# Kernel tuning notes

Measured on AMD Instinct MI355X. Metric: run time of the kernel, lower is better.

The kernel has to match this reference:

```python
import jax, jax.numpy as jnp
import numpy as np

BN_EPS = 1e-5
NORM_EPS = 1e-12  # torch F.normalize eps


def setup_inputs() -> dict:
    key = jax.random.key(0)
    k0, k1, k2 = jax.random.split(key, 3)
    B, C, H, W, M = 16, 256, 64, 64, 512
    query = jax.random.normal(k0, (B, C, H, W), jnp.float32)
    mem = jax.random.normal(k1, (M, C), jnp.float32)
    mem = mem / jnp.maximum(jnp.linalg.norm(mem, axis=1, keepdims=True), NORM_EPS)
    conv_w = jax.random.normal(k2, (256, 2 * C), jnp.float32) * 0.02  # 1x1 conv: [out, in]
    bn_gamma = jnp.ones((256,), jnp.float32)
    bn_beta = jnp.zeros((256,), jnp.float32)
    return {"query": query, "mem": mem, "conv_w": conv_w,
            "bn_gamma": bn_gamma, "bn_beta": bn_beta}


def reference(query, mem, conv_w, bn_gamma, bn_beta):
    B, C, H, W = query.shape
    # F.normalize over channel dim
    q = query / jnp.maximum(jnp.linalg.norm(query, axis=1, keepdims=True), NORM_EPS)
    # permute(0,2,3,1) then flatten -> [N, C], N = B*H*W
    q = q.transpose(0, 2, 3, 1).reshape(B * H * W, C)
    # query-memory similarity [N, M]
    score = q @ mem.T
    softmax_score_query = jax.nn.softmax(score, axis=0)   # softmax over all queries
    softmax_score_memory = jax.nn.softmax(score, axis=1)  # softmax over memory slots
    # weighted read from memory bank (scores detached in original)
    concat_memory = jax.lax.stop_gradient(softmax_score_memory) @ mem  # [N, C]
    updated = jnp.concatenate([q, concat_memory], axis=1)              # [N, 2C]
    updated = updated.reshape(B, H, W, 2 * C).transpose(0, 3, 1, 2)    # [B, 2C, H, W]
    # 1x1 conv (bias=False)
    y = jnp.einsum('oc,bchw->bohw', conv_w, updated)
    # BatchNorm2d (training-mode batch statistics) + ReLU
    mean = y.mean(axis=(0, 2, 3), keepdims=True)
    var = y.var(axis=(0, 2, 3), keepdims=True)
    y = (y - mean) * jax.lax.rsqrt(var + BN_EPS)
    y = y * bn_gamma[None, :, None, None] + bn_beta[None, :, None, None]
    y = jnp.maximum(y, 0.0)
    return y, softmax_score_query, softmax_score_memory
```

## Files before the change

kernel.cpp:

```cpp
#include <hip/hip_runtime.h>
#include <math.h>

#define Bq 16
#define Cc 256
#define HW 4096
#define Mm 512
#define Nn 65536
#define Oo 256
#define Kf 768

typedef short bf16x8 __attribute__((ext_vector_type(8)));
typedef float f32x4 __attribute__((ext_vector_type(4)));
typedef unsigned short ushort_t;

__device__ __forceinline__ unsigned int bf16rne(float f) {
  unsigned int u = __float_as_uint(f);
  return (u + 0x7FFFu + ((u >> 16) & 1u)) >> 16;
}
__device__ __forceinline__ float bf16f(unsigned int h) { return __uint_as_float(h << 16); }
__device__ __forceinline__ void split2(float v0, float v1,
                                       unsigned int& hi, unsigned int& lo) {
  unsigned int h0 = bf16rne(v0), h1 = bf16rne(v1);
  hi = h0 | (h1 << 16);
  unsigned int l0 = bf16rne(v0 - bf16f(h0)), l1 = bf16rne(v1 - bf16f(h1));
  lo = l0 | (l1 << 16);
}

__global__ __launch_bounds__(256) void k_qt(const float* __restrict__ query,
                                            ushort_t* __restrict__ qhiT,
                                            ushort_t* __restrict__ qloT,
                                            const float* __restrict__ mem,
                                            ushort_t* __restrict__ memT) {
  __shared__ float T[256][36];
  __shared__ float S2[8][32];
  __shared__ float invn_s[32];
  int tid = threadIdx.x, bid = blockIdx.x;
  if (bid < 2048) {
    int n0 = bid * 32;
    int b = n0 >> 12, hw0 = n0 & 4095;
    const float* qb = query + (size_t)b * Cc * HW + hw0;
#pragma unroll
    for (int p = 0; p < 8; ++p) {
      int idx = p * 256 + tid;
      int c = idx >> 3, f4 = idx & 7;
      float4 v = *(const float4*)(qb + (size_t)c * HW + f4 * 4);
      *(float4*)&T[c][f4 * 4] = v;
    }
    __syncthreads();
    {
      int n = tid & 31, cq = tid >> 5;
      float s = 0.f;
#pragma unroll
      for (int c = 0; c < 32; ++c) { float v = T[cq * 32 + c][n]; s += v * v; }
      S2[cq][n] = s;
    }
    __syncthreads();
    if (tid < 32) {
      float s = 0.f;
#pragma unroll
      for (int q = 0; q < 8; ++q) s += S2[q][tid];
      invn_s[tid] = 1.f / fmaxf(sqrtf(s), 1e-12f);
    }
    __syncthreads();
#pragma unroll
    for (int p = 0; p < 4; ++p) {
      int idx = p * 256 + tid;
      int n = idx & 31, g = idx >> 5;
      float ivn = invn_s[n];
      unsigned int hv[4], lv[4];
#pragma unroll
      for (int h = 0; h < 4; ++h) {
        int c0 = g * 8 + h * 2;
        split2(T[c0][n] * ivn, T[c0 + 1][n] * ivn, hv[h], lv[h]);
      }
      *(uint4*)(qhiT + (size_t)(n0 + n) * 256 + g * 8) = make_uint4(hv[0], hv[1], hv[2], hv[3]);
      *(uint4*)(qloT + (size_t)(n0 + n) * 256 + g * 8) = make_uint4(lv[0], lv[1], lv[2], lv[3]);
    }
  } else {
    int r0 = (bid - 2048) * 64;
#pragma unroll
    for (int p = 0; p < 8; ++p) {
      int idx = p * 256 + tid;
      int row = idx >> 5, g = idx & 31;
      const float* src = mem + (size_t)(r0 + row) * 256 + g * 8;
      float4 a = *(const float4*)(src);
      float4 c = *(const float4*)(src + 4);
      unsigned int w0 = bf16rne(a.x) | (bf16rne(a.y) << 16);
      unsigned int w1 = bf16rne(a.z) | (bf16rne(a.w) << 16);
      unsigned int w2 = bf16rne(c.x) | (bf16rne(c.y) << 16);
      unsigned int w3 = bf16rne(c.z) | (bf16rne(c.w) << 16);
      *(uint4*)(memT + (size_t)(r0 + row) * 256 + g * 8) = make_uint4(w0, w1, w2, w3);
    }
  }
}

__global__ __launch_bounds__(256) void k_wm(const float* __restrict__ conv_w,
                                            const float* __restrict__ mem,
                                            ushort_t* __restrict__ Ahi,
                                            ushort_t* __restrict__ Alo) {
  __shared__ __align__(16) float Asm[16 * 132];
  __shared__ __align__(16) float Bsm[16 * 132];
  int tid = threadIdx.x, bid = blockIdx.x;
  if (bid >= 8) {
    int b8 = bid - 8;
#pragma unroll
    for (int p = 0; p < 8; ++p) {
      int idx = b8 * 2048 + p * 256 + tid;
      int o = idx >> 6, c4 = (idx & 63) * 4;
      float4 v = *(const float4*)(conv_w + (size_t)o * 512 + c4);
      unsigned int h0, l0, h1, l1;
      split2(v.x, v.y, h0, l0);
      split2(v.z, v.w, h1, l1);
      *(uint2*)(Ahi + (size_t)o * 768 + c4) = make_uint2(h0, h1);
      *(uint2*)(Alo + (size_t)o * 768 + c4) = make_uint2(l0, l1);
    }
    return;
  }
  int tile_o = bid & 1, tile_m = bid >> 1;
  int o0 = tile_o * 128, m0 = tile_m * 128;
  int tx = tid & 15, ty = tid >> 4;
  int akk = tid & 15, ao0 = tid >> 4;
  int bk = tid & 15, bm = tid >> 4;

  float acc[2][2][4][4];
#pragma unroll
  for (int a = 0; a < 2; ++a)
#pragma unroll
    for (int c = 0; c < 2; ++c)
#pragma unroll
      for (int i = 0; i < 4; ++i)
#pragma unroll
        for (int j = 0; j < 4; ++j) acc[a][c][i][j] = 0.f;

  for (int k0 = 0; k0 < Cc; k0 += 16) {
#pragma unroll
    for (int i = 0; i < 8; ++i) {
      int o = ao0 + i * 16;
      Asm[akk * 132 + o] = conv_w[(size_t)(o0 + o) * 512 + 256 + k0 + akk];
    }
#pragma unroll
    for (int i = 0; i < 8; ++i) {
      int m = bm + i * 16;
      Bsm[bk * 132 + m] = mem[(size_t)(m0 + m) * Cc + k0 + bk];
    }
    __syncthreads();
#pragma unroll
    for (int kk = 0; kk < 16; ++kk) {
      float4 a0 = *(const float4*)&Asm[kk * 132 + ty * 4];
      float4 a1 = *(const float4*)&Asm[kk * 132 + 64 + ty * 4];
      float4 b0 = *(const float4*)&Bsm[kk * 132 + tx * 4];
      float4 b1 = *(const float4*)&Bsm[kk * 132 + 64 + tx * 4];
      float av[2][4] = {{a0.x, a0.y, a0.z, a0.w}, {a1.x, a1.y, a1.z, a1.w}};
      float bv[2][4] = {{b0.x, b0.y, b0.z, b0.w}, {b1.x, b1.y, b1.z, b1.w}};
#pragma unroll
      for (int ib = 0; ib < 2; ++ib)
#pragma unroll
        for (int i = 0; i < 4; ++i)
#pragma unroll
          for (int jb = 0; jb < 2; ++jb)
#pragma unroll
            for (int j = 0; j < 4; ++j) acc[ib][jb][i][j] += av[ib][i] * bv[jb][j];
    }
    __syncthreads();
  }
#pragma unroll
  for (int ib = 0; ib < 2; ++ib)
#pragma unroll
    for (int i = 0; i < 4; ++i) {
      int o = o0 + ib * 64 + ty * 4 + i;
#pragma unroll
      for (int jb = 0; jb < 2; ++jb) {
        int mc = m0 + jb * 64 + tx * 4;
        unsigned int h0, l0, h1, l1;
        split2(acc[ib][jb][i][0], acc[ib][jb][i][1], h0, l0);
        split2(acc[ib][jb][i][2], acc[ib][jb][i][3], h1, l1);
        *(uint2*)(Ahi + (size_t)o * 768 + 256 + mc) = make_uint2(h0, h1);
        *(uint2*)(Alo + (size_t)o * 768 + 256 + mc) = make_uint2(l0, l1);
      }
    }
}

__global__ __launch_bounds__(256) void k_score(const ushort_t* __restrict__ qhiT,
                                               const ushort_t* __restrict__ memT,
                                               float* __restrict__ exs,
                                               float* __restrict__ rowsum,
                                               float* __restrict__ colsum) {
  __shared__ ushort_t As[128 * 64];
  __shared__ ushort_t Bs[128 * 64];
  int tid = threadIdx.x, bid = blockIdx.x;
  int m0 = (bid & 3) * 128;
  int n0 = (bid >> 2) * 128;
  int lane = tid & 63;
  int w = tid >> 6, wrow = w >> 1, wcol = w & 1;

  f32x4 acc[4][4];
#pragma unroll
  for (int i = 0; i < 4; ++i)
#pragma unroll
    for (int j = 0; j < 4; ++j)
#pragma unroll
      for (int e = 0; e < 4; ++e) acc[i][j][e] = 0.f;

  uint4* As4 = (uint4*)As;
  uint4* Bs4 = (uint4*)Bs;

  for (int kt = 0; kt < 4; ++kt) {
    int k0 = kt * 64;
#pragma unroll
    for (int p = 0; p < 4; ++p) {
      int idx = p * 256 + tid;
      int row = idx >> 3, g = idx & 7;
      int G = g ^ (row & 7);
      As4[row * 8 + G] = *(const uint4*)(qhiT + (size_t)(n0 + row) * 256 + k0 + g * 8);
      Bs4[row * 8 + G] = *(const uint4*)(memT + (size_t)(m0 + row) * 256 + k0 + g * 8);
    }
    __syncthreads();
#pragma unroll
    for (int ks = 0; ks < 2; ++ks) {
      bf16x8 a[4], b[4];
#pragma unroll
      for (int i = 0; i < 4; ++i) {
        int row = wrow * 64 + i * 16 + (lane & 15);
        int G = ((lane >> 4) + ks * 4) ^ (row & 7);
        a[i] = ((const bf16x8*)As)[row * 8 + G];
      }
#pragma unroll
      for (int j = 0; j < 4; ++j) {
        int row = wcol * 64 + j * 16 + (lane & 15);
        int G = ((lane >> 4) + ks * 4) ^ (row & 7);
        b[j] = ((const bf16x8*)Bs)[row * 8 + G];
      }
#pragma unroll
      for (int i = 0; i < 4; ++i)
#pragma unroll
        for (int j = 0; j < 4; ++j)
          acc[i][j] = __builtin_amdgcn_mfma_f32_16x16x32_bf16(a[i], b[j], acc[i][j], 0, 0, 0);
    }
    __syncthreads();
  }

  float rp[4][4], cp[4];
#pragma unroll
  for (int i = 0; i < 4; ++i)
#pragma unroll
    for (int r = 0; r < 4; ++r) rp[i][r] = 0.f;
#pragma unroll
  for (int j = 0; j < 4; ++j) cp[j] = 0.f;

#pragma unroll
  for (int i = 0; i < 4; ++i) {
#pragma unroll
    for (int r = 0; r < 4; ++r) {
      int pl = wrow * 64 + i * 16 + (lane >> 4) * 4 + r;
      float* orow = exs + (size_t)(n0 + pl) * Mm + m0;
#pragma unroll
      for (int j = 0; j < 4; ++j) {
        int sl = wcol * 64 + j * 16 + (lane & 15);
        float e = __expf(acc[i][j][r]);
        orow[sl] = e;
        rp[i][r] += e;
        cp[j] += e;
      }
    }
  }

  float* red = (float*)As;
#pragma unroll
  for (int i = 0; i < 4; ++i)
#pragma unroll
    for (int r = 0; r < 4; ++r) {
      int pl = wrow * 64 + i * 16 + (lane >> 4) * 4 + r;
      red[pl * 32 + wcol * 16 + (lane & 15)] = rp[i][r];
    }
  __syncthreads();
  if (tid < 128) {
    float s = 0.f;
#pragma unroll
    for (int x = 0; x < 32; ++x) s += red[tid * 32 + x];
    atomicAdd(&rowsum[n0 + tid], s);
  }
  __syncthreads();
#pragma unroll
  for (int j = 0; j < 4; ++j) {
    int sl = wcol * 64 + j * 16 + (lane & 15);
    red[sl * 8 + wrow * 4 + (lane >> 4)] = cp[j];
  }
  __syncthreads();
  if (tid < 128) {
    float s = 0.f;
#pragma unroll
    for (int x = 0; x < 8; ++x) s += red[tid * 8 + x];
    atomicAdd(&colsum[m0 + tid], s);
  }
}

__global__ __launch_bounds__(256) void k_conv(const ushort_t* __restrict__ Ahi,
                                              const ushort_t* __restrict__ Alo,
                                              const ushort_t* __restrict__ qhiT,
                                              const ushort_t* __restrict__ qloT,
                                              const float* __restrict__ exs,
                                              const float* __restrict__ rowsum,
                                              float* __restrict__ y,
                                              float* __restrict__ bnsum,
                                              float* __restrict__ bnsumsq) {
  __shared__ ushort_t AsH[128 * 64], AsL[128 * 64];
  __shared__ ushort_t BsH[128 * 64], BsL[128 * 64];
  __shared__ float irow[128];
  int tid = threadIdx.x, bid = blockIdx.x;
  int tile_o = bid & 1, tile_n = bid >> 1;
  int o0 = tile_o * 128, n0 = tile_n * 128;
  int b = n0 >> 12, hw0 = n0 & 4095;
  if (tid < 128) irow[tid] = 1.0f / rowsum[n0 + tid];
  int lane = tid & 63;
  int w = tid >> 6, wrow = w >> 1, wcol = w & 1;

  f32x4 acc[4][4];
#pragma unroll
  for (int i = 0; i < 4; ++i)
#pragma unroll
    for (int j = 0; j < 4; ++j)
#pragma unroll
      for (int e = 0; e < 4; ++e) acc[i][j][e] = 0.f;

  uint4* AsH4 = (uint4*)AsH;
  uint4* AsL4 = (uint4*)AsL;
  uint4* BsH4 = (uint4*)BsH;
  uint4* BsL4 = (uint4*)BsL;
  uint2* BsH2 = (uint2*)BsH;
  uint2* BsL2 = (uint2*)BsL;
  __syncthreads();

  for (int kt = 0; kt < 12; ++kt) {
    int k0 = kt * 64;
#pragma unroll
    for (int p = 0; p < 4; ++p) {
      int idx = p * 256 + tid;
      int row = idx >> 3, g = idx & 7;
      int G = g ^ (row & 7);
      size_t src = (size_t)(o0 + row) * 768 + k0 + g * 8;
      AsH4[row * 8 + G] = *(const uint4*)(Ahi + src);
      AsL4[row * 8 + G] = *(const uint4*)(Alo + src);
    }
    if (k0 < 256) {
#pragma unroll
      for (int p = 0; p < 4; ++p) {
        int idx = p * 256 + tid;
        int row = idx >> 3, g = idx & 7;
        int G = g ^ (row & 7);
        size_t src = (size_t)(n0 + row) * 256 + k0 + g * 8;
        BsH4[row * 8 + G] = *(const uint4*)(qhiT + src);
        BsL4[row * 8 + G] = *(const uint4*)(qloT + src);
      }
    } else {
#pragma unroll
      for (int p = 0; p < 8; ++p) {
        int idx = p * 256 + tid;
        int row = idx >> 4, f4 = idx & 15;
        float ir = irow[row];
        float4 v = *(const float4*)(exs + (size_t)(n0 + row) * Mm + (k0 - 256) + f4 * 4);
        unsigned int h0, l0, h1, l1;
        split2(v.x * ir, v.y * ir, h0, l0);
        split2(v.z * ir, v.w * ir, h1, l1);
        int g = f4 >> 1, half = f4 & 1;
        int G = g ^ (row & 7);
        BsH2[(row * 8 + G) * 2 + half] = make_uint2(h0, h1);
        BsL2[(row * 8 + G) * 2 + half] = make_uint2(l0, l1);
      }
    }
    __syncthreads();
#pragma unroll
    for (int ks = 0; ks < 2; ++ks) {
      bf16x8 ah[4], al[4], bh[4], bl[4];
#pragma unroll
      for (int i = 0; i < 4; ++i) {
        int row = wrow * 64 + i * 16 + (lane & 15);
        int G = ((lane >> 4) + ks * 4) ^ (row & 7);
        ah[i] = ((const bf16x8*)AsH)[row * 8 + G];
        al[i] = ((const bf16x8*)AsL)[row * 8 + G];
      }
#pragma unroll
      for (int j = 0; j < 4; ++j) {
        int row = wcol * 64 + j * 16 + (lane & 15);
        int G = ((lane >> 4) + ks * 4) ^ (row & 7);
        bh[j] = ((const bf16x8*)BsH)[row * 8 + G];
        bl[j] = ((const bf16x8*)BsL)[row * 8 + G];
      }
#pragma unroll
      for (int i = 0; i < 4; ++i)
#pragma unroll
        for (int j = 0; j < 4; ++j) {
          acc[i][j] = __builtin_amdgcn_mfma_f32_16x16x32_bf16(al[i], bh[j], acc[i][j], 0, 0, 0);
          acc[i][j] = __builtin_amdgcn_mfma_f32_16x16x32_bf16(ah[i], bl[j], acc[i][j], 0, 0, 0);
          acc[i][j] = __builtin_amdgcn_mfma_f32_16x16x32_bf16(ah[i], bh[j], acc[i][j], 0, 0, 0);
        }
    }
    __syncthreads();
  }

  float rp[4][4], rq[4][4];
#pragma unroll
  for (int i = 0; i < 4; ++i)
#pragma unroll
    for (int r = 0; r < 4; ++r) { rp[i][r] = 0.f; rq[i][r] = 0.f; }

#pragma unroll
  for (int i = 0; i < 4; ++i) {
#pragma unroll
    for (int r = 0; r < 4; ++r) {
      int pl = wrow * 64 + i * 16 + (lane >> 4) * 4 + r;
      float* orow = y + (size_t)b * Oo * HW + (size_t)(o0 + pl) * HW + hw0;
#pragma unroll
      for (int j = 0; j < 4; ++j) {
        int sl = wcol * 64 + j * 16 + (lane & 15);
        float v = acc[i][j][r];
        orow[sl] = v;
        rp[i][r] += v;
        rq[i][r] += v * v;
      }
    }
  }

  float* red = (float*)AsH;
#pragma unroll
  for (int i = 0; i < 4; ++i)
#pragma unroll
    for (int r = 0; r < 4; ++r) {
      int pl = wrow * 64 + i * 16 + (lane >> 4) * 4 + r;
      red[pl * 32 + wcol * 16 + (lane & 15)] = rp[i][r];
    }
  __syncthreads();
  if (tid < 128) {
    float s = 0.f;
#pragma unroll
    for (int x = 0; x < 32; ++x) s += red[tid * 32 + x];
    atomicAdd(&bnsum[o0 + tid], s);
  }
  __syncthreads();
#pragma unroll
  for (int i = 0; i < 4; ++i)
#pragma unroll
    for (int r = 0; r < 4; ++r) {
      int pl = wrow * 64 + i * 16 + (lane >> 4) * 4 + r;
      red[pl * 32 + wcol * 16 + (lane & 15)] = rq[i][r];
    }
  __syncthreads();
  if (tid < 128) {
    float s = 0.f;
#pragma unroll
    for (int x = 0; x < 32; ++x) s += red[tid * 32 + x];
    atomicAdd(&bnsumsq[o0 + tid], s);
  }
}

__global__ __launch_bounds__(256) void k_final(float4* __restrict__ y4,
                                               const float* __restrict__ bnsum,
                                               const float* __restrict__ bnsumsq,
                                               const float* __restrict__ gamma,
                                               const float* __restrict__ beta,
                                               float4* __restrict__ smm4,
                                               const float* __restrict__ rowsum,
                                               const float4* __restrict__ colsum4,
                                               float4* __restrict__ smq4) {
  int bid = blockIdx.x;
  if (bid < 16384) {
    int g = bid * 256 + threadIdx.x;
    int o = (g >> 10) & 255;
    float mean = bnsum[o] * (1.f / Nn);
    float var = bnsumsq[o] * (1.f / Nn) - mean * mean;
    float s = gamma[o] * rsqrtf(var + 1e-5f);
    float t = beta[o] - mean * s;
    float4 v = y4[g];
    v.x = fmaxf(v.x * s + t, 0.f);
    v.y = fmaxf(v.y * s + t, 0.f);
    v.z = fmaxf(v.z * s + t, 0.f);
    v.w = fmaxf(v.w * s + t, 0.f);
    y4[g] = v;
  } else {
    int g = (bid - 16384) * 256 + threadIdx.x;
    int n = g >> 7;
    int c4 = g & 127;
    float4 e = smm4[g];
    float4 cs = colsum4[c4];
    float irn = 1.0f / rowsum[n];
    smq4[g] = make_float4(e.x / cs.x, e.y / cs.y, e.z / cs.z, e.w / cs.w);
    smm4[g] = make_float4(e.x * irn, e.y * irn, e.z * irn, e.w * irn);
  }
}

extern "C" void kernel_launch(void* const* d_in, const int* in_sizes, int n_in,
                              void* d_out, int out_size, void* d_ws, size_t ws_size,
                              hipStream_t stream) {
  (void)in_sizes; (void)n_in; (void)out_size; (void)ws_size;
  const float* query  = (const float*)d_in[0];
  const float* mem    = (const float*)d_in[1];
  const float* conv_w = (const float*)d_in[2];
  const float* gamma  = (const float*)d_in[3];
  const float* beta   = (const float*)d_in[4];
  float* out = (float*)d_out;
  float* y   = out;
  float* smq = out + 16777216;
  float* smm = smq + 33554432;
  ushort_t* qhiT = (ushort_t*)smq;
  ushort_t* qloT = (ushort_t*)(smq + 8388608);
  ushort_t* memT = (ushort_t*)(smq + 16777216);
  ushort_t* Ahi  = (ushort_t*)(smq + 16842752);
  ushort_t* Alo  = (ushort_t*)(smq + 16941056);
  float* ws = (float*)d_ws;
  float* rowsum  = ws;
  float* colsum  = ws + 65536;
  float* bnsum   = ws + 66048;
  float* bnsumsq = ws + 66304;

  hipMemsetAsync(ws, 0, 66560 * sizeof(float), stream);

  k_qt<<<2056, 256, 0, stream>>>(query, qhiT, qloT, mem, memT);
  k_wm<<<16, 256, 0, stream>>>(conv_w, mem, Ahi, Alo);
  k_score<<<2048, 256, 0, stream>>>(qhiT, memT, smm, rowsum, colsum);
  k_conv<<<1024, 256, 0, stream>>>(Ahi, Alo, qhiT, qloT, smm, rowsum,
                                   y, bnsum, bnsumsq);
  k_final<<<49152, 256, 0, stream>>>((float4*)y, bnsum, bnsumsq, gamma, beta,
                                     (float4*)smm, rowsum,
                                     (const float4*)colsum, (float4*)smq);
}
```

Baseline: 593.8 us.

## Fuse softmax normalization into conv kernel and load MFMA operands directly from global

Intermediates (exp scores, bf16 splits) move from the output buffer into workspace. Both softmax outputs are now written inside the conv kernel (only the tile_o==0 blocks) while it is already reading the exp scores. The final kernel is reduced to the BN+ReLU pass. This removes a separate full read/write pass over the two 128 MB softmax arrays. The score kernel and the q/A operand loads in the conv kernel skip LDS staging and read bf16x8 fragments straight from global memory, which drops barriers but relies on caches for operand reuse. The launcher now returns early if the workspace is too small.

Result: slower. 702.2 us (+18.3%).

```diff
diff --git a/kernel.cpp b/kernel.cpp
--- a/kernel.cpp
+++ b/kernel.cpp
@@ -7,11 +7,22 @@
 #define Mm 512
 #define Nn 65536
 #define Oo 256
-#define Kf 768
 
 typedef short bf16x8 __attribute__((ext_vector_type(8)));
 typedef float f32x4 __attribute__((ext_vector_type(4)));
 typedef unsigned short ushort_t;
+
+#define WS_ROWSUM  0
+#define WS_COLSUM  65536
+#define WS_BNSUM   66048
+#define WS_BNSUMSQ 66304
+#define WS_EXS     66560
+#define WS_QHI     33620992
+#define WS_QLO     42009600
+#define WS_MEMT    50398208
+#define WS_AHI     50463744
+#define WS_ALO     50562048
+#define WS_TOTAL   50660352
 
 __device__ __forceinline__ unsigned int bf16rne(float f) {
   unsigned int u = __float_as_uint(f);
@@ -185,13 +196,13 @@
                                                float* __restrict__ exs,
                                                float* __restrict__ rowsum,
                                                float* __restrict__ colsum) {
-  __shared__ ushort_t As[128 * 64];
-  __shared__ ushort_t Bs[128 * 64];
+  __shared__ float red[128 * 32];
   int tid = threadIdx.x, bid = blockIdx.x;
   int m0 = (bid & 3) * 128;
   int n0 = (bid >> 2) * 128;
   int lane = tid & 63;
   int w = tid >> 6, wrow = w >> 1, wcol = w & 1;
+  int rlane = lane & 15, klane = (lane >> 4) * 8;
 
   f32x4 acc[4][4];
 #pragma unroll
@@ -201,42 +212,26 @@
 #pragma unroll
       for (int e = 0; e < 4; ++e) acc[i][j][e] = 0.f;
 
-  uint4* As4 = (uint4*)As;
-  uint4* Bs4 = (uint4*)Bs;
+  const ushort_t* qbase = qhiT + (size_t)(n0 + wrow * 64 + rlane) * 256 + klane;
+  const ushort_t* mbase = memT + (size_t)(m0 + wcol * 64 + rlane) * 256 + klane;
 
   for (int kt = 0; kt < 4; ++kt) {
-    int k0 = kt * 64;
-#pragma unroll
-    for (int p = 0; p < 4; ++p) {
-      int idx = p * 256 + tid;
-      int row = idx >> 3, g = idx & 7;
-      int G = g ^ (row & 7);
-      As4[row * 8 + G] = *(const uint4*)(qhiT + (size_t)(n0 + row) * 256 + k0 + g * 8);
-      Bs4[row * 8 + G] = *(const uint4*)(memT + (size_t)(m0 + row) * 256 + k0 + g * 8);
-    }
-    __syncthreads();
 #pragma unroll
     for (int ks = 0; ks < 2; ++ks) {
+      int k0 = kt * 64 + ks * 32;
       bf16x8 a[4], b[4];
 #pragma unroll
-      for (int i = 0; i < 4; ++i) {
-        int row = wrow * 64 + i * 16 + (lane & 15);
-        int G = ((lane >> 4) + ks * 4) ^ (row & 7);
-        a[i] = ((const bf16x8*)As)[row * 8 + G];
-      }
-#pragma unroll
-      for (int j = 0; j < 4; ++j) {
-        int row = wcol * 64 + j * 16 + (lane & 15);
-        int G = ((lane >> 4) + ks * 4) ^ (row & 7);
-        b[j] = ((const bf16x8*)Bs)[row * 8 + G];
-      }
+      for (int i = 0; i < 4; ++i)
+        a[i] = *(const bf16x8*)(qbase + (size_t)(i * 16) * 256 + k0);
+#pragma unroll
+      for (int j = 0; j < 4; ++j)
+        b[j] = *(const bf16x8*)(mbase + (size_t)(j * 16) * 256 + k0);
 #pragma unroll
       for (int i = 0; i < 4; ++i)
 #pragma unroll
         for (int j = 0; j < 4; ++j)
           acc[i][j] = __builtin_amdgcn_mfma_f32_16x16x32_bf16(a[i], b[j], acc[i][j], 0, 0, 0);
     }
-    __syncthreads();
   }
 
   float rp[4][4], cp[4];
@@ -264,7 +259,6 @@
     }
   }
 
-  float* red = (float*)As;
 #pragma unroll
   for (int i = 0; i < 4; ++i)
 #pragma unroll
@@ -300,19 +294,25 @@
                                               const ushort_t* __restrict__ qloT,
                                               const float* __restrict__ exs,
                                               const float* __restrict__ rowsum,
+                                              const float* __restrict__ colsum,
                                               float* __restrict__ y,
+                                              float* __restrict__ smm,
+                                              float* __restrict__ smq,
                                               float* __restrict__ bnsum,
                                               float* __restrict__ bnsumsq) {
-  __shared__ ushort_t AsH[128 * 64], AsL[128 * 64];
   __shared__ ushort_t BsH[128 * 64], BsL[128 * 64];
   __shared__ float irow[128];
+  __shared__ float invc[512];
   int tid = threadIdx.x, bid = blockIdx.x;
   int tile_o = bid & 1, tile_n = bid >> 1;
   int o0 = tile_o * 128, n0 = tile_n * 128;
   int b = n0 >> 12, hw0 = n0 & 4095;
   if (tid < 128) irow[tid] = 1.0f / rowsum[n0 + tid];
+  invc[tid] = 1.0f / colsum[tid];
+  invc[tid + 256] = 1.0f / colsum[tid + 256];
   int lane = tid & 63;
   int w = tid >> 6, wrow = w >> 1, wcol = w & 1;
+  int rlane = lane & 15, klane = (lane >> 4) * 8;
 
   f32x4 acc[4][4];
 #pragma unroll
@@ -322,61 +322,74 @@
 #pragma unroll
       for (int e = 0; e < 4; ++e) acc[i][j][e] = 0.f;
 
-  uint4* AsH4 = (uint4*)AsH;
-  uint4* AsL4 = (uint4*)AsL;
-  uint4* BsH4 = (uint4*)BsH;
-  uint4* BsL4 = (uint4*)BsL;
+  const ushort_t* ahB = Ahi + (size_t)(o0 + wrow * 64 + rlane) * 768 + klane;
+  const ushort_t* alB = Alo + (size_t)(o0 + wrow * 64 + rlane) * 768 + klane;
+  const ushort_t* qhB = qhiT + (size_t)(n0 + wcol * 64 + rlane) * 256 + klane;
+  const ushort_t* qlB = qloT + (size_t)(n0 + wcol * 64 + rlane) * 256 + klane;
   uint2* BsH2 = (uint2*)BsH;
   uint2* BsL2 = (uint2*)BsL;
   __syncthreads();
 
-  for (int kt = 0; kt < 12; ++kt) {
-    int k0 = kt * 64;
-#pragma unroll
-    for (int p = 0; p < 4; ++p) {
+  for (int kt = 0; kt < 4; ++kt) {
+#pragma unroll
+    for (int ks = 0; ks < 2; ++ks) {
+      int k0 = kt * 64 + ks * 32;
+      bf16x8 ah[4], al[4], bh[4], bl[4];
+#pragma unroll
+      for (int i = 0; i < 4; ++i) {
+        ah[i] = *(const bf16x8*)(ahB + (size_t)(i * 16) * 768 + k0);
+        al[i] = *(const bf16x8*)(alB + (size_t)(i * 16) * 768 + k0);
+      }
+#pragma unroll
+      for (int j = 0; j < 4; ++j) {
+        bh[j] = *(const bf16x8*)(qhB + (size_t)(j * 16) * 256 + k0);
+        bl[j] = *(const bf16x8*)(qlB + (size_t)(j * 16) * 256 + k0);
+      }
+#pragma unroll
+      for (int i = 0; i < 4; ++i)
+#pragma unroll
+        for (int j = 0; j < 4; ++j) {
+          acc[i][j] = __builtin_amdgcn_mfma_f32_16x16x32_bf16(al[i], bh[j], acc[i][j], 0, 0, 0);
+          acc[i][j] = __builtin_amdgcn_mfma_f32_16x16x32_bf16(ah[i], bl[j], acc[i][j], 0, 0, 0);
+          acc[i][j] = __builtin_amdgcn_mfma_f32_16x16x32_bf16(ah[i], bh[j], acc[i][j], 0, 0, 0);
+        }
+    }
+  }
+
+  for (int kt2 = 0; kt2 < 8; ++kt2) {
+    int kg = 256 + kt2 * 64;
+    int kc = kt2 * 64;
+#pragma unroll
+    for (int p = 0; p < 8; ++p) {
       int idx = p * 256 + tid;
-      int row = idx >> 3, g = idx & 7;
+      int row = idx >> 4, f4 = idx & 15;
+      int col = kc + f4 * 4;
+      float ir = irow[row];
+      float4 v = *(const float4*)(exs + (size_t)(n0 + row) * Mm + col);
+      float4 pv = make_float4(v.x * ir, v.y * ir, v.z * ir, v.w * ir);
+      if (tile_o == 0) {
+        *(float4*)(smm + (size_t)(n0 + row) * Mm + col) = pv;
+        float4 ic = *(const float4*)&invc[col];
+        *(float4*)(smq + (size_t)(n0 + row) * Mm + col) =
+            make_float4(v.x * ic.x, v.y * ic.y, v.z * ic.z, v.w * ic.w);
+      }
+      unsigned int h0, l0, h1, l1;
+      split2(pv.x, pv.y, h0, l0);
+      split2(pv.z, pv.w, h1, l1);
+      int g = f4 >> 1, half = f4 & 1;
       int G = g ^ (row & 7);
-      size_t src = (size_t)(o0 + row) * 768 + k0 + g * 8;
-      AsH4[row * 8 + G] = *(const uint4*)(Ahi + src);
-      AsL4[row * 8 + G] = *(const uint4*)(Alo + src);
-    }
-    if (k0 < 256) {
-#pragma unroll
-      for (int p = 0; p < 4; ++p) {
-        int idx = p * 256 + tid;
-        int row = idx >> 3, g = idx & 7;
-        int G = g ^ (row & 7);
-        size_t src = (size_t)(n0 + row) * 256 + k0 + g * 8;
-        BsH4[row * 8 + G] = *(const uint4*)(qhiT + src);
-        BsL4[row * 8 + G] = *(const uint4*)(qloT + src);
-      }
-    } else {
-#pragma unroll
-      for (int p = 0; p < 8; ++p) {
-        int idx = p * 256 + tid;
-        int row = idx >> 4, f4 = idx & 15;
-        float ir = irow[row];
-        float4 v = *(const float4*)(exs + (size_t)(n0 + row) * Mm + (k0 - 256) + f4 * 4);
-        unsigned int h0, l0, h1, l1;
-        split2(v.x * ir, v.y * ir, h0, l0);
-        split2(v.z * ir, v.w * ir, h1, l1);
-        int g = f4 >> 1, half = f4 & 1;
-        int G = g ^ (row & 7);
-        BsH2[(row * 8 + G) * 2 + half] = make_uint2(h0, h1);
-        BsL2[(row * 8 + G) * 2 + half] = make_uint2(l0, l1);
-      }
+      BsH2[(row * 8 + G) * 2 + half] = make_uint2(h0, h1);
+      BsL2[(row * 8 + G) * 2 + half] = make_uint2(l0, l1);
     }
     __syncthreads();
 #pragma unroll
     for (int ks = 0; ks < 2; ++ks) {
+      int k0 = kg + ks * 32;
       bf16x8 ah[4], al[4], bh[4], bl[4];
 #pragma unroll
       for (int i = 0; i < 4; ++i) {
-        int row = wrow * 64 + i * 16 + (lane & 15);
-        int G = ((lane >> 4) + ks * 4) ^ (row & 7);
-        ah[i] = ((const bf16x8*)AsH)[row * 8 + G];
-        al[i] = ((const bf16x8*)AsL)[row * 8 + G];
+        ah[i] = *(const bf16x8*)(ahB + (size_t)(i * 16) * 768 + k0);
+        al[i] = *(const bf16x8*)(alB + (size_t)(i * 16) * 768 + k0);
       }
 #pragma unroll
       for (int j = 0; j < 4; ++j) {
@@ -420,7 +433,7 @@
     }
   }
 
-  float* red = (float*)AsH;
+  float* red = (float*)BsH;
 #pragma unroll
   for (int i = 0; i < 4; ++i)
 #pragma unroll
@@ -452,45 +465,30 @@
   }
 }
 
-__global__ __launch_bounds__(256) void k_final(float4* __restrict__ y4,
-                                               const float* __restrict__ bnsum,
-                                               const float* __restrict__ bnsumsq,
-                                               const float* __restrict__ gamma,
-                                               const float* __restrict__ beta,
-                                               float4* __restrict__ smm4,
-                                               const float* __restrict__ rowsum,
-                                               const float4* __restrict__ colsum4,
-                                               float4* __restrict__ smq4) {
-  int bid = blockIdx.x;
-  if (bid < 16384) {
-    int g = bid * 256 + threadIdx.x;
-    int o = (g >> 10) & 255;
-    float mean = bnsum[o] * (1.f / Nn);
-    float var = bnsumsq[o] * (1.f / Nn) - mean * mean;
-    float s = gamma[o] * rsqrtf(var + 1e-5f);
-    float t = beta[o] - mean * s;
-    float4 v = y4[g];
-    v.x = fmaxf(v.x * s + t, 0.f);
-    v.y = fmaxf(v.y * s + t, 0.f);
-    v.z = fmaxf(v.z * s + t, 0.f);
-    v.w = fmaxf(v.w * s + t, 0.f);
-    y4[g] = v;
-  } else {
-    int g = (bid - 16384) * 256 + threadIdx.x;
-    int n = g >> 7;
-    int c4 = g & 127;
-    float4 e = smm4[g];
-    float4 cs = colsum4[c4];
-    float irn = 1.0f / rowsum[n];
-    smq4[g] = make_float4(e.x / cs.x, e.y / cs.y, e.z / cs.z, e.w / cs.w);
-    smm4[g] = make_float4(e.x * irn, e.y * irn, e.z * irn, e.w * irn);
-  }
+__global__ __launch_bounds__(256) void k_final_y(float4* __restrict__ y4,
+                                                 const float* __restrict__ bnsum,
+                                                 const float* __restrict__ bnsumsq,
+                                                 const float* __restrict__ gamma,
+                                                 const float* __restrict__ beta) {
+  int g = blockIdx.x * 256 + threadIdx.x;
+  int o = (g >> 10) & 255;
+  float mean = bnsum[o] * (1.f / Nn);
+  float var = bnsumsq[o] * (1.f / Nn) - mean * mean;
+  float s = gamma[o] * rsqrtf(var + 1e-5f);
+  float t = beta[o] - mean * s;
+  float4 v = y4[g];
+  v.x = fmaxf(v.x * s + t, 0.f);
+  v.y = fmaxf(v.y * s + t, 0.f);
+  v.z = fmaxf(v.z * s + t, 0.f);
+  v.w = fmaxf(v.w * s + t, 0.f);
+  y4[g] = v;
 }
 
 extern "C" void kernel_launch(void* const* d_in, const int* in_sizes, int n_in,
                               void* d_out, int out_size, void* d_ws, size_t ws_size,
                               hipStream_t stream) {
-  (void)in_sizes; (void)n_in; (void)out_size; (void)ws_size;
+  (void)in_sizes; (void)n_in; (void)out_size;
+  if (ws_size < (size_t)WS_TOTAL * sizeof(float)) return;
   const float* query  = (const float*)d_in[0];
   const float* mem    = (const float*)d_in[1];
   const float* conv_w = (const float*)d_in[2];
@@ -500,25 +498,24 @@
   float* y   = out;
   float* smq = out + 16777216;
   float* smm = smq + 33554432;
-  ushort_t* qhiT = (ushort_t*)smq;
-  ushort_t* qloT = (ushort_t*)(smq + 8388608);
-  ushort_t* memT = (ushort_t*)(smq + 16777216);
-  ushort_t* Ahi  = (ushort_t*)(smq + 16842752);
-  ushort_t* Alo  = (ushort_t*)(smq + 16941056);
   float* ws = (float*)d_ws;
-  float* rowsum  = ws;
-  float* colsum  = ws + 65536;
-  float* bnsum   = ws + 66048;
-  float* bnsumsq = ws + 66304;
+  float* rowsum  = ws + WS_ROWSUM;
+  float* colsum  = ws + WS_COLSUM;
+  float* bnsum   = ws + WS_BNSUM;
+  float* bnsumsq = ws + WS_BNSUMSQ;
+  float* exs     = ws + WS_EXS;
+  ushort_t* qhiT = (ushort_t*)(ws + WS_QHI);
+  ushort_t* qloT = (ushort_t*)(ws + WS_QLO);
+  ushort_t* memT = (ushort_t*)(ws + WS_MEMT);
+  ushort_t* Ahi  = (ushort_t*)(ws + WS_AHI);
+  ushort_t* Alo  = (ushort_t*)(ws + WS_ALO);
 
   hipMemsetAsync(ws, 0, 66560 * sizeof(float), stream);
 
   k_qt<<<2056, 256, 0, stream>>>(query, qhiT, qloT, mem, memT);
   k_wm<<<16, 256, 0, stream>>>(conv_w, mem, Ahi, Alo);
-  k_score<<<2048, 256, 0, stream>>>(qhiT, memT, smm, rowsum, colsum);
-  k_conv<<<1024, 256, 0, stream>>>(Ahi, Alo, qhiT, qloT, smm, rowsum,
-                                   y, bnsum, bnsumsq);
-  k_final<<<49152, 256, 0, stream>>>((float4*)y, bnsum, bnsumsq, gamma, beta,
-                                     (float4*)smm, rowsum,
-                                     (const float4*)colsum, (float4*)smq);
-}
+  k_score<<<2048, 256, 0, stream>>>(qhiT, memT, exs, rowsum, colsum);
+  k_conv<<<1024, 256, 0, stream>>>(Ahi, Alo, qhiT, qloT, exs, rowsum, colsum,
+                                   y, smm, smq, bnsum, bnsumsq);
+  k_final_y<<<16384, 256, 0, stream>>>((float4*)y, bnsum, bnsumsq, gamma, beta);
+}
```
